# Kernel optimization log

Measured on AMD Instinct MI355X. Metric: run time of the kernel, lower is better.

The kernel has to match this reference:

```python
import jax, jax.numpy as jnp
import numpy as np

HIDDEN = 2048
NUM_HEADS = 16
HEAD_DIM = 128
OUT = NUM_HEADS * HEAD_DIM  # 2048
B, T = 4, 2048


def setup_inputs() -> dict:
    key = jax.random.key(0)
    ks = jax.random.split(key, 8)
    hidden_states = jax.random.normal(ks[0], (B, T, HIDDEN), dtype=jnp.float32)
    scale = 0.02
    Wr = jax.random.normal(ks[1], (OUT, HIDDEN), dtype=jnp.float32) * scale
    Wk = jax.random.normal(ks[2], (OUT, HIDDEN), dtype=jnp.float32) * scale
    Wv = jax.random.normal(ks[3], (OUT, HIDDEN), dtype=jnp.float32) * scale
    Wo = jax.random.normal(ks[4], (HIDDEN, OUT), dtype=jnp.float32) * scale
    time_decay = jax.random.uniform(ks[5], (NUM_HEADS, HEAD_DIM), minval=-4.0, maxval=-1.0, dtype=jnp.float32)
    time_first = jax.random.uniform(ks[6], (NUM_HEADS, HEAD_DIM), minval=-0.5, maxval=0.5, dtype=jnp.float32)
    time_mix_k = jnp.full((1, 1, HIDDEN), 0.5, dtype=jnp.float32)
    time_mix_v = jnp.full((1, 1, HIDDEN), 0.5, dtype=jnp.float32)
    time_mix_r = jnp.full((1, 1, HIDDEN), 0.5, dtype=jnp.float32)
    return {"hidden_states": hidden_states, "Wr": Wr, "Wk": Wk, "Wv": Wv, "Wo": Wo,
            "time_decay": time_decay, "time_first": time_first,
            "time_mix_k": time_mix_k, "time_mix_v": time_mix_v, "time_mix_r": time_mix_r}


def _wkv(r, k, v, time_decay, time_first):
    # r,k,v: [B,T,H,D] -> output [B,T,H,D]
    w = jnp.exp(-jnp.exp(time_decay))  # [H,D]
    u = time_first                     # [H,D]
    kv = k * v                         # [B,T,H,D]
    # scan over time: carry state [B,H,D]
    r_t = jnp.moveaxis(r, 1, 0)   # [T,B,H,D]
    kv_t = jnp.moveaxis(kv, 1, 0)

    def step(state, inp):
        rt, kvt = inp
        out = (state + u * kvt) * rt
        new_state = state * w + kvt
        return new_state, out

    state0 = jnp.zeros(r.shape[:1] + r.shape[2:], dtype=r.dtype)  # [B,H,D]
    _, out = jax.lax.scan(step, state0, (r_t, kv_t))
    return jnp.moveaxis(out, 0, 1)  # [B,T,H,D]


def reference(hidden_states, Wr, Wk, Wv, Wo, time_decay, time_first, time_mix_k, time_mix_v, time_mix_r):
    Bc, Tc, _ = hidden_states.shape
    # token shift: xx[t] = hidden[t-1], xx[0] = 0
    xx = jnp.concatenate([jnp.zeros_like(hidden_states[:, :1]), hidden_states[:, :-1]], axis=1)
    xk = hidden_states * time_mix_k + xx * (1.0 - time_mix_k)
    xv = hidden_states * time_mix_v + xx * (1.0 - time_mix_v)
    xr = hidden_states * time_mix_r + xx * (1.0 - time_mix_r)
    receptance = jax.nn.sigmoid(jnp.einsum('bth,oh->bto', xr, Wr))
    key = jnp.einsum('bth,oh->bto', xk, Wk)
    value = jnp.einsum('bth,oh->bto', xv, Wv)
    receptance = receptance.reshape(Bc, Tc, NUM_HEADS, HEAD_DIM)
    key = key.reshape(Bc, Tc, NUM_HEADS, HEAD_DIM)
    value = value.reshape(Bc, Tc, NUM_HEADS, HEAD_DIM)
    wkv = _wkv(receptance, key, value, time_decay, time_first)
    attn = wkv.reshape(Bc, Tc, OUT)
    return jnp.einsum('bto,ho->bth', attn, Wo)
```

## Files before the change

kernel.cpp:

```cpp
#include <hip/hip_runtime.h>


#define HIDDEN 2048
#define TOUT   2048
#define TT     2048
#define MM     8192

typedef __bf16 bf16_t;
typedef __attribute__((ext_vector_type(8))) __bf16 bf16x8;
typedef __attribute__((ext_vector_type(4))) __bf16 bf16x4;
typedef __attribute__((ext_vector_type(4))) float  f32x4;

__global__ __launch_bounds__(256) void f2bf_kernel(const float* __restrict__ src,
                                                   bf16_t* __restrict__ dst) {
  const long i = ((long)blockIdx.x * 256 + threadIdx.x) * 4;
  const float4 v = *reinterpret_cast<const float4*>(src + i);
  bf16x4 o;
  o[0] = (bf16_t)v.x; o[1] = (bf16_t)v.y; o[2] = (bf16_t)v.z; o[3] = (bf16_t)v.w;
  *reinterpret_cast<bf16x4*>(dst + i) = o;
}

__global__ __launch_bounds__(256) void prep_kernel(const float* __restrict__ h,
    const float* __restrict__ mk, const float* __restrict__ mv,
    const float* __restrict__ mr,
    bf16_t* __restrict__ xk, bf16_t* __restrict__ xv, bf16_t* __restrict__ xr) {
  const long i  = ((long)blockIdx.x * 256 + threadIdx.x) * 4;
  const int  c  = (int)(i & (HIDDEN - 1));
  const long bt = i >> 11;
  const int  t  = (int)(bt & (TT - 1));
  const float4 hv = *reinterpret_cast<const float4*>(h + i);
  float4 hp = make_float4(0.f, 0.f, 0.f, 0.f);
  if (t > 0) hp = *reinterpret_cast<const float4*>(h + i - HIDDEN);
  const float4 k4 = *reinterpret_cast<const float4*>(mk + c);
  const float4 v4 = *reinterpret_cast<const float4*>(mv + c);
  const float4 r4 = *reinterpret_cast<const float4*>(mr + c);
  bf16x4 ok, ov, orr;
#define MIX(j, HC, PC)                                         \
  ok[j]  = (bf16_t)(HC * k4.PC + hp.PC * (1.f - k4.PC));       \
  ov[j]  = (bf16_t)(HC * v4.PC + hp.PC * (1.f - v4.PC));       \
  orr[j] = (bf16_t)(HC * r4.PC + hp.PC * (1.f - r4.PC));
  MIX(0, hv.x, x) MIX(1, hv.y, y) MIX(2, hv.z, z) MIX(3, hv.w, w)
#undef MIX
  *reinterpret_cast<bf16x4*>(xk + i) = ok;
  *reinterpret_cast<bf16x4*>(xv + i) = ov;
  *reinterpret_cast<bf16x4*>(xr + i) = orr;
}

#define GBM 256
#define GBN 256
#define GBK 64

template<bool SIGMOID, bool OUTF32>
__global__ __launch_bounds__(512, 2) void gemm256(const bf16_t* __restrict__ A,
                                                  const bf16_t* __restrict__ W,
                                                  bf16_t* __restrict__ Cb,
                                                  float* __restrict__ Cf) {
  __shared__ __align__(16) char lds[131072];
  const int tid = threadIdx.x, wave = tid >> 6, lane = tid & 63;
  const int wr = wave >> 2, wc = wave & 3;
  const long rowA0 = (long)blockIdx.x * GBM;
  const long rowB0 = (long)blockIdx.y * GBN;
  const bf16_t* aB = A + rowA0 * HIDDEN;
  const bf16_t* wB = W + rowB0 * HIDDEN;

  const int sgofs = (wave * 8 + (lane >> 3)) * HIDDEN + (((lane & 7) ^ (lane >> 3)) << 3);
  const int ldst  = wave * 1024;

#define STAGE(J, BUFX) do {                                                     \
    const int kt_ = (J) * GBK;                                                  \
    _Pragma("unroll")                                                           \
    for (int i_ = 0; i_ < 4; ++i_) {                                            \
      __builtin_amdgcn_global_load_lds(                                         \
        (const __attribute__((address_space(1))) void*)(aB + sgofs + i_ * (64 * HIDDEN) + kt_), \
        (__attribute__((address_space(3))) void*)(lds + (BUFX) + ldst + i_ * 8192), 16, 0, 0);  \
      __builtin_amdgcn_global_load_lds(                                         \
        (const __attribute__((address_space(1))) void*)(wB + sgofs + i_ * (64 * HIDDEN) + kt_), \
        (__attribute__((address_space(3))) void*)(lds + 65536 + (BUFX) + ldst + i_ * 8192), 16, 0, 0); \
    } } while (0)

  const int rsel = lane & 15, g0 = lane >> 4;
  int offA[8], offB[4];
#pragma unroll
  for (int m = 0; m < 8; ++m) {
    const int row = wr * 128 + m * 16 + rsel;
    offA[m] = row * 128 + ((g0 ^ (row & 7)) << 4);
  }
#pragma unroll
  for (int n = 0; n < 4; ++n) {
    const int row = wc * 64 + n * 16 + rsel;
    offB[n] = 65536 + row * 128 + ((g0 ^ (row & 7)) << 4);
  }

  f32x4 acc[8][4];
#pragma unroll
  for (int m = 0; m < 8; ++m)
#pragma unroll
    for (int n = 0; n < 4; ++n)
#pragma unroll
      for (int q = 0; q < 4; ++q) acc[m][n][q] = 0.f;

  STAGE(0, 0);
  STAGE(1, 32768);

  int bufx = 0;
  for (int j = 0; j < 32; ++j) {
    if (j < 31) { asm volatile("s_waitcnt vmcnt(8)" ::: "memory"); }
    else        { asm volatile("s_waitcnt vmcnt(0)" ::: "memory"); }
    __builtin_amdgcn_sched_barrier(0);
    __builtin_amdgcn_s_barrier();

    bf16x8 a0[8], b0[4], a1[8], b1[4];
#pragma unroll
    for (int m = 0; m < 8; ++m) a0[m] = *reinterpret_cast<const bf16x8*>(lds + (offA[m] ^ bufx));
#pragma unroll
    for (int n = 0; n < 4; ++n) b0[n] = *reinterpret_cast<const bf16x8*>(lds + (offB[n] ^ bufx));
    __builtin_amdgcn_s_setprio(1);
#pragma unroll
    for (int m = 0; m < 8; ++m)
#pragma unroll
      for (int n = 0; n < 4; ++n)
        acc[m][n] = __builtin_amdgcn_mfma_f32_16x16x32_bf16(a0[m], b0[n], acc[m][n], 0, 0, 0);
    __builtin_amdgcn_s_setprio(0);
#pragma unroll
    for (int m = 0; m < 8; ++m) a1[m] = *reinterpret_cast<const bf16x8*>(lds + (offA[m] ^ bufx ^ 64));
#pragma unroll
    for (int n = 0; n < 4; ++n) b1[n] = *reinterpret_cast<const bf16x8*>(lds + (offB[n] ^ bufx ^ 64));
    asm volatile("s_waitcnt lgkmcnt(0)" ::: "memory");
    __builtin_amdgcn_sched_barrier(0);
    __builtin_amdgcn_s_barrier();
    if (j < 30) STAGE(j + 2, bufx);
    __builtin_amdgcn_s_setprio(1);
#pragma unroll
    for (int m = 0; m < 8; ++m)
#pragma unroll
      for (int n = 0; n < 4; ++n)
        acc[m][n] = __builtin_amdgcn_mfma_f32_16x16x32_bf16(a1[m], b1[n], acc[m][n], 0, 0, 0);
    __builtin_amdgcn_s_setprio(0);
    bufx ^= 32768;
  }
#undef STAGE

  const long crow0 = rowA0 + wr * 128 + g0 * 4;
  const long ccol0 = rowB0 + wc * 64 + rsel;
#pragma unroll
  for (int m = 0; m < 8; ++m) {
#pragma unroll
    for (int n = 0; n < 4; ++n) {
#pragma unroll
      for (int q = 0; q < 4; ++q) {
        float val = acc[m][n][q];
        if (SIGMOID) val = 1.f / (1.f + __expf(-val));
        const long row = crow0 + m * 16 + q;
        const long col = ccol0 + n * 16;
        if (OUTF32) Cf[row * TOUT + col] = val;
        else        Cb[row * TOUT + col] = (bf16_t)val;
      }
    }
  }
}

#define CL  64
#define NCH 32

__global__ __launch_bounds__(256) void wkv_state_kernel(
    const bf16_t* __restrict__ kp, const bf16_t* __restrict__ vp,
    const float* __restrict__ td, float* __restrict__ cs ) {
  const int c8 = blockIdx.x * 256 + threadIdx.x;
  const int ch = blockIdx.y;
  const int o0 = (c8 * 8) & (TOUT - 1);
  const int b  = c8 >> 8;
  const long base = ((long)b * TT + ch * CL) * TOUT + o0;
  float w[8], s[8];
#pragma unroll
  for (int i = 0; i < 8; ++i) { w[i] = __expf(-__expf(td[o0 + i])); s[i] = 0.f; }
  for (int t = 0; t < CL; ++t) {
    const bf16x8 k8 = *reinterpret_cast<const bf16x8*>(kp + base + (long)t * TOUT);
    const bf16x8 v8 = *reinterpret_cast<const bf16x8*>(vp + base + (long)t * TOUT);
#pragma unroll
    for (int i = 0; i < 8; ++i) s[i] = s[i] * w[i] + (float)k8[i] * (float)v8[i];
  }
  float4* csv = reinterpret_cast<float4*>(cs + ch * MM + c8 * 8);
  csv[0] = make_float4(s[0], s[1], s[2], s[3]);
  csv[1] = make_float4(s[4], s[5], s[6], s[7]);
}

__global__ __launch_bounds__(256) void wkv_out_kernel(
    const bf16_t* __restrict__ rp, const bf16_t* __restrict__ kp,
    const bf16_t* __restrict__ vp, const float* __restrict__ td,
    const float* __restrict__ tf, const float* __restrict__ cs,
    bf16_t* __restrict__ attn) {
  const int c8 = blockIdx.x * 256 + threadIdx.x;
  const int ch = blockIdx.y;
  const int o0 = (c8 * 8) & (TOUT - 1);
  const int b  = c8 >> 8;
  const long base = ((long)b * TT + ch * CL) * TOUT + o0;
  float w[8], u[8], wc[8], S[8];
#pragma unroll
  for (int i = 0; i < 8; ++i) {
    const float e = __expf(td[o0 + i]);
    w[i]  = __expf(-e);
    wc[i] = __expf(-e * (float)CL);
    u[i]  = tf[o0 + i];
    S[i]  = 0.f;
  }
  for (int j2 = 0; j2 < ch; ++j2) {
    const float4 s0 = *reinterpret_cast<const float4*>(cs + j2 * MM + c8 * 8);
    const float4 s1 = *reinterpret_cast<const float4*>(cs + j2 * MM + c8 * 8 + 4);
    S[0] = S[0] * wc[0] + s0.x; S[1] = S[1] * wc[1] + s0.y;
    S[2] = S[2] * wc[2] + s0.z; S[3] = S[3] * wc[3] + s0.w;
    S[4] = S[4] * wc[4] + s1.x; S[5] = S[5] * wc[5] + s1.y;
    S[6] = S[6] * wc[6] + s1.z; S[7] = S[7] * wc[7] + s1.w;
  }
  for (int t = 0; t < CL; ++t) {
    const bf16x8 r8 = *reinterpret_cast<const bf16x8*>(rp + base + (long)t * TOUT);
    const bf16x8 k8 = *reinterpret_cast<const bf16x8*>(kp + base + (long)t * TOUT);
    const bf16x8 v8 = *reinterpret_cast<const bf16x8*>(vp + base + (long)t * TOUT);
    bf16x8 o8;
#pragma unroll
    for (int i = 0; i < 8; ++i) {
      const float kv = (float)k8[i] * (float)v8[i];
      o8[i] = (bf16_t)((S[i] + u[i] * kv) * (float)r8[i]);
      S[i] = S[i] * w[i] + kv;
    }
    *reinterpret_cast<bf16x8*>(attn + base + (long)t * TOUT) = o8;
  }
}

extern "C" void kernel_launch(void* const* d_in, const int* in_sizes, int n_in,
                              void* d_out, int out_size, void* d_ws, size_t ws_size,
                              hipStream_t stream) {
  const float* h  = (const float*)d_in[0];
  const float* Wr = (const float*)d_in[1];
  const float* Wk = (const float*)d_in[2];
  const float* Wv = (const float*)d_in[3];
  const float* Wo = (const float*)d_in[4];
  const float* td = (const float*)d_in[5];
  const float* tf = (const float*)d_in[6];
  const float* mk = (const float*)d_in[7];
  const float* mv = (const float*)d_in[8];
  const float* mr = (const float*)d_in[9];
  float* out = (float*)d_out;

  char* ws = (char*)d_ws;
  const size_t S2 = (size_t)MM * TOUT * sizeof(bf16_t);
  bf16_t* xr   = (bf16_t*)(ws + 0 * S2);
  bf16_t* xk   = (bf16_t*)(ws + 1 * S2);
  bf16_t* xv   = (bf16_t*)(ws + 2 * S2);
  bf16_t* rr   = (bf16_t*)(ws + 3 * S2);
  bf16_t* kk   = (bf16_t*)(ws + 4 * S2);
  bf16_t* vv   = xr;
  bf16_t* attn = xk;
  float*  cs   = (float*)xv;
  const size_t WSZ = (size_t)TOUT * HIDDEN;
  bf16_t* Wr2 = (bf16_t*)(ws + 5 * S2);
  bf16_t* Wk2 = Wr2 + WSZ;
  bf16_t* Wv2 = Wk2 + WSZ;
  bf16_t* Wo2 = Wv2 + WSZ;

  f2bf_kernel<<<4096, 256, 0, stream>>>(Wr, Wr2);
  f2bf_kernel<<<4096, 256, 0, stream>>>(Wk, Wk2);
  f2bf_kernel<<<4096, 256, 0, stream>>>(Wv, Wv2);
  f2bf_kernel<<<4096, 256, 0, stream>>>(Wo, Wo2);

  prep_kernel<<<16384, 256, 0, stream>>>(h, mk, mv, mr, xk, xv, xr);

  dim3 gg(MM / GBM, TOUT / GBN);
  gemm256<true , false><<<gg, 512, 0, stream>>>(xr, Wr2, rr, nullptr);
  gemm256<false, false><<<gg, 512, 0, stream>>>(xk, Wk2, kk, nullptr);
  gemm256<false, false><<<gg, 512, 0, stream>>>(xv, Wv2, vv, nullptr);

  dim3 wg(4, NCH);
  wkv_state_kernel<<<wg, 256, 0, stream>>>(kk, vv, td, cs);
  wkv_out_kernel<<<wg, 256, 0, stream>>>(rr, kk, vv, td, tf, cs, attn);

  gemm256<false, true ><<<gg, 512, 0, stream>>>(attn, Wo2, nullptr, out);
}
```

Baseline: 490.5 us.

## Restructure GEMM mainloop into four-phase interleaved load/MFMA schedule; merge weight casts

The GEMM main loop is rebuilt as four sub-phases per K-tile. Each phase loads a quarter of the A/B fragments from LDS, issues half of an operand's global-to-LDS prefetch, and runs 16 MFMAs. This spreads memory traffic across the MFMA work instead of issuing it in two large bursts. The four weight-cast launches are merged into one 2D-grid kernel, and both the cast and prep kernels now process 8 elements per thread. The finer schedule adds more barriers per iteration and relies on hand-tuned vmcnt/lgkmcnt counts that must match the issued loads exactly.

```diff
diff --git a/kernel.cpp b/kernel.cpp
--- a/kernel.cpp
+++ b/kernel.cpp
@@ -5,45 +5,66 @@
 #define TOUT   2048
 #define TT     2048
 #define MM     8192
+#define NT     32
 
 typedef __bf16 bf16_t;
 typedef __attribute__((ext_vector_type(8))) __bf16 bf16x8;
-typedef __attribute__((ext_vector_type(4))) __bf16 bf16x4;
 typedef __attribute__((ext_vector_type(4))) float  f32x4;
 
-__global__ __launch_bounds__(256) void f2bf_kernel(const float* __restrict__ src,
-                                                   bf16_t* __restrict__ dst) {
-  const long i = ((long)blockIdx.x * 256 + threadIdx.x) * 4;
-  const float4 v = *reinterpret_cast<const float4*>(src + i);
-  bf16x4 o;
-  o[0] = (bf16_t)v.x; o[1] = (bf16_t)v.y; o[2] = (bf16_t)v.z; o[3] = (bf16_t)v.w;
-  *reinterpret_cast<bf16x4*>(dst + i) = o;
+__global__ __launch_bounds__(256) void f2bf4_kernel(
+    const float* __restrict__ s0, const float* __restrict__ s1,
+    const float* __restrict__ s2, const float* __restrict__ s3,
+    bf16_t* __restrict__ d0, bf16_t* __restrict__ d1,
+    bf16_t* __restrict__ d2, bf16_t* __restrict__ d3) {
+  const float* s; bf16_t* d;
+  switch (blockIdx.y) {
+    case 0:  s = s0; d = d0; break;
+    case 1:  s = s1; d = d1; break;
+    case 2:  s = s2; d = d2; break;
+    default: s = s3; d = d3; break;
+  }
+  const long i = ((long)blockIdx.x * 256 + threadIdx.x) * 8;
+  const float4 a = *reinterpret_cast<const float4*>(s + i);
+  const float4 b = *reinterpret_cast<const float4*>(s + i + 4);
+  bf16x8 o;
+  o[0] = (bf16_t)a.x; o[1] = (bf16_t)a.y; o[2] = (bf16_t)a.z; o[3] = (bf16_t)a.w;
+  o[4] = (bf16_t)b.x; o[5] = (bf16_t)b.y; o[6] = (bf16_t)b.z; o[7] = (bf16_t)b.w;
+  *reinterpret_cast<bf16x8*>(d + i) = o;
 }
 
 __global__ __launch_bounds__(256) void prep_kernel(const float* __restrict__ h,
     const float* __restrict__ mk, const float* __restrict__ mv,
     const float* __restrict__ mr,
     bf16_t* __restrict__ xk, bf16_t* __restrict__ xv, bf16_t* __restrict__ xr) {
-  const long i  = ((long)blockIdx.x * 256 + threadIdx.x) * 4;
-  const int  c  = (int)(i & (HIDDEN - 1));
-  const long bt = i >> 11;
-  const int  t  = (int)(bt & (TT - 1));
-  const float4 hv = *reinterpret_cast<const float4*>(h + i);
-  float4 hp = make_float4(0.f, 0.f, 0.f, 0.f);
-  if (t > 0) hp = *reinterpret_cast<const float4*>(h + i - HIDDEN);
-  const float4 k4 = *reinterpret_cast<const float4*>(mk + c);
-  const float4 v4 = *reinterpret_cast<const float4*>(mv + c);
-  const float4 r4 = *reinterpret_cast<const float4*>(mr + c);
-  bf16x4 ok, ov, orr;
-#define MIX(j, HC, PC)                                         \
-  ok[j]  = (bf16_t)(HC * k4.PC + hp.PC * (1.f - k4.PC));       \
-  ov[j]  = (bf16_t)(HC * v4.PC + hp.PC * (1.f - v4.PC));       \
-  orr[j] = (bf16_t)(HC * r4.PC + hp.PC * (1.f - r4.PC));
-  MIX(0, hv.x, x) MIX(1, hv.y, y) MIX(2, hv.z, z) MIX(3, hv.w, w)
-#undef MIX
-  *reinterpret_cast<bf16x4*>(xk + i) = ok;
-  *reinterpret_cast<bf16x4*>(xv + i) = ov;
-  *reinterpret_cast<bf16x4*>(xr + i) = orr;
+  const long i = ((long)blockIdx.x * 256 + threadIdx.x) * 8;
+  const int  c = (int)(i & (HIDDEN - 1));
+  const int  t = (int)((i >> 11) & (TT - 1));
+  float hv[8], hp[8], k8[8], v8[8], r8[8];
+  *reinterpret_cast<float4*>(hv)     = *reinterpret_cast<const float4*>(h + i);
+  *reinterpret_cast<float4*>(hv + 4) = *reinterpret_cast<const float4*>(h + i + 4);
+  if (t > 0) {
+    *reinterpret_cast<float4*>(hp)     = *reinterpret_cast<const float4*>(h + i - HIDDEN);
+    *reinterpret_cast<float4*>(hp + 4) = *reinterpret_cast<const float4*>(h + i - HIDDEN + 4);
+  } else {
+#pragma unroll
+    for (int j = 0; j < 8; ++j) hp[j] = 0.f;
+  }
+  *reinterpret_cast<float4*>(k8)     = *reinterpret_cast<const float4*>(mk + c);
+  *reinterpret_cast<float4*>(k8 + 4) = *reinterpret_cast<const float4*>(mk + c + 4);
+  *reinterpret_cast<float4*>(v8)     = *reinterpret_cast<const float4*>(mv + c);
+  *reinterpret_cast<float4*>(v8 + 4) = *reinterpret_cast<const float4*>(mv + c + 4);
+  *reinterpret_cast<float4*>(r8)     = *reinterpret_cast<const float4*>(mr + c);
+  *reinterpret_cast<float4*>(r8 + 4) = *reinterpret_cast<const float4*>(mr + c + 4);
+  bf16x8 ok, ov, orr;
+#pragma unroll
+  for (int j = 0; j < 8; ++j) {
+    ok[j]  = (bf16_t)(hv[j] * k8[j] + hp[j] * (1.f - k8[j]));
+    ov[j]  = (bf16_t)(hv[j] * v8[j] + hp[j] * (1.f - v8[j]));
+    orr[j] = (bf16_t)(hv[j] * r8[j] + hp[j] * (1.f - r8[j]));
+  }
+  *reinterpret_cast<bf16x8*>(xk + i) = ok;
+  *reinterpret_cast<bf16x8*>(xv + i) = ov;
+  *reinterpret_cast<bf16x8*>(xr + i) = orr;
 }
 
 #define GBM 256
@@ -66,16 +87,15 @@
   const int sgofs = (wave * 8 + (lane >> 3)) * HIDDEN + (((lane & 7) ^ (lane >> 3)) << 3);
   const int ldst  = wave * 1024;
 
-#define STAGE(J, BUFX) do {                                                     \
-    const int kt_ = (J) * GBK;                                                  \
+#define STAGE_H(J, OP, HALF) do {                                               \
+    const int j_ = (J);                                                         \
+    const bf16_t* s_ = (OP) ? wB : aB;                                          \
+    const int lb_ = ((OP) ? 65536 : 0) + ((j_ & 1) << 15) + ldst;               \
     _Pragma("unroll")                                                           \
-    for (int i_ = 0; i_ < 4; ++i_) {                                            \
+    for (int i_ = 2 * (HALF); i_ < 2 * (HALF) + 2; ++i_) {                      \
       __builtin_amdgcn_global_load_lds(                                         \
-        (const __attribute__((address_space(1))) void*)(aB + sgofs + i_ * (64 * HIDDEN) + kt_), \
-        (__attribute__((address_space(3))) void*)(lds + (BUFX) + ldst + i_ * 8192), 16, 0, 0);  \
-      __builtin_amdgcn_global_load_lds(                                         \
-        (const __attribute__((address_space(1))) void*)(wB + sgofs + i_ * (64 * HIDDEN) + kt_), \
-        (__attribute__((address_space(3))) void*)(lds + 65536 + (BUFX) + ldst + i_ * 8192), 16, 0, 0); \
+        (const __attribute__((address_space(1))) void*)(s_ + sgofs + i_ * (64 * HIDDEN) + j_ * GBK), \
+        (__attribute__((address_space(3))) void*)(lds + lb_ + i_ * 8192), 16, 0, 0); \
     } } while (0)
 
   const int rsel = lane & 15, g0 = lane >> 4;
@@ -99,46 +119,64 @@
 #pragma unroll
       for (int q = 0; q < 4; ++q) acc[m][n][q] = 0.f;
 
-  STAGE(0, 0);
-  STAGE(1, 32768);
-
-  int bufx = 0;
-  for (int j = 0; j < 32; ++j) {
-    if (j < 31) { asm volatile("s_waitcnt vmcnt(8)" ::: "memory"); }
-    else        { asm volatile("s_waitcnt vmcnt(0)" ::: "memory"); }
+#define LD(off) (*reinterpret_cast<const bf16x8*>(lds + (off)))
+#define MFMA16(AR, M0, BR, N0) do {                                             \
+    __builtin_amdgcn_s_setprio(1);                                              \
+    _Pragma("unroll")                                                           \
+    for (int m_ = 0; m_ < 4; ++m_)                                              \
+      _Pragma("unroll")                                                         \
+      for (int n_ = 0; n_ < 2; ++n_)                                            \
+        _Pragma("unroll")                                                       \
+        for (int s_ = 0; s_ < 2; ++s_)                                          \
+          acc[(M0) + m_][(N0) + n_] = __builtin_amdgcn_mfma_f32_16x16x32_bf16(  \
+              AR[m_][s_], BR[n_][s_], acc[(M0) + m_][(N0) + n_], 0, 0, 0);      \
+    __builtin_amdgcn_s_setprio(0); } while (0)
+#define PH_SYNC() do {                                                          \
+    __builtin_amdgcn_s_barrier();                                               \
+    asm volatile("s_waitcnt lgkmcnt(0)" ::: "memory");                          \
+    __builtin_amdgcn_sched_barrier(0); } while (0)
+
+  STAGE_H(0, 0, 0); STAGE_H(0, 0, 1); STAGE_H(0, 1, 0); STAGE_H(0, 1, 1);
+  STAGE_H(1, 0, 0); STAGE_H(1, 0, 1);
+  asm volatile("s_waitcnt vmcnt(4)" ::: "memory");
+  __builtin_amdgcn_s_barrier();
+
+  for (int j = 0; j < NT; ++j) {
+    const int bufx = (j & 1) << 15;
+    bf16x8 aR0[4][2], aR1[4][2], bR0[2][2], bR1[2][2];
+#pragma unroll
+    for (int m = 0; m < 4; ++m) { aR0[m][0] = LD(offA[m] ^ bufx); aR0[m][1] = LD(offA[m] ^ bufx ^ 64); }
+#pragma unroll
+    for (int n = 0; n < 2; ++n) { bR0[n][0] = LD(offB[n] ^ bufx); bR0[n][1] = LD(offB[n] ^ bufx ^ 64); }
+    if (j + 1 < NT) STAGE_H(j + 1, 1, 0);
+    asm volatile("s_waitcnt lgkmcnt(8)" ::: "memory");
+    PH_SYNC();
+    MFMA16(aR0, 0, bR0, 0);
+    __builtin_amdgcn_s_barrier();
+#pragma unroll
+    for (int m = 0; m < 4; ++m) { aR1[m][0] = LD(offA[4 + m] ^ bufx); aR1[m][1] = LD(offA[4 + m] ^ bufx ^ 64); }
+    if (j + 1 < NT) STAGE_H(j + 1, 1, 1);
+    PH_SYNC();
+    MFMA16(aR1, 4, bR0, 0);
+    __builtin_amdgcn_s_barrier();
+#pragma unroll
+    for (int n = 0; n < 2; ++n) { bR1[n][0] = LD(offB[2 + n] ^ bufx); bR1[n][1] = LD(offB[2 + n] ^ bufx ^ 64); }
+    if (j + 2 < NT) STAGE_H(j + 2, 0, 0);
+    PH_SYNC();
+    MFMA16(aR1, 4, bR1, 2);
+    __builtin_amdgcn_s_barrier();
+    if (j + 2 < NT) STAGE_H(j + 2, 0, 1);
+    if (j <= NT - 3)      { asm volatile("s_waitcnt vmcnt(4)" ::: "memory"); }
+    else if (j == NT - 2) { asm volatile("s_waitcnt vmcnt(0)" ::: "memory"); }
     __builtin_amdgcn_sched_barrier(0);
+    PH_SYNC();
+    MFMA16(aR0, 0, bR1, 2);
     __builtin_amdgcn_s_barrier();
-
-    bf16x8 a0[8], b0[4], a1[8], b1[4];
-#pragma unroll
-    for (int m = 0; m < 8; ++m) a0[m] = *reinterpret_cast<const bf16x8*>(lds + (offA[m] ^ bufx));
-#pragma unroll
-    for (int n = 0; n < 4; ++n) b0[n] = *reinterpret_cast<const bf16x8*>(lds + (offB[n] ^ bufx));
-    __builtin_amdgcn_s_setprio(1);
-#pragma unroll
-    for (int m = 0; m < 8; ++m)
-#pragma unroll
-      for (int n = 0; n < 4; ++n)
-        acc[m][n] = __builtin_amdgcn_mfma_f32_16x16x32_bf16(a0[m], b0[n], acc[m][n], 0, 0, 0);
-    __builtin_amdgcn_s_setprio(0);
-#pragma unroll
-    for (int m = 0; m < 8; ++m) a1[m] = *reinterpret_cast<const bf16x8*>(lds + (offA[m] ^ bufx ^ 64));
-#pragma unroll
-    for (int n = 0; n < 4; ++n) b1[n] = *reinterpret_cast<const bf16x8*>(lds + (offB[n] ^ bufx ^ 64));
-    asm volatile("s_waitcnt lgkmcnt(0)" ::: "memory");
-    __builtin_amdgcn_sched_barrier(0);
-    __builtin_amdgcn_s_barrier();
-    if (j < 30) STAGE(j + 2, bufx);
-    __builtin_amdgcn_s_setprio(1);
-#pragma unroll
-    for (int m = 0; m < 8; ++m)
-#pragma unroll
-      for (int n = 0; n < 4; ++n)
-        acc[m][n] = __builtin_amdgcn_mfma_f32_16x16x32_bf16(a1[m], b1[n], acc[m][n], 0, 0, 0);
-    __builtin_amdgcn_s_setprio(0);
-    bufx ^= 32768;
-  }
-#undef STAGE
+  }
+#undef STAGE_H
+#undef LD
+#undef MFMA16
+#undef PH_SYNC
 
   const long crow0 = rowA0 + wr * 128 + g0 * 4;
   const long ccol0 = rowB0 + wc * 64 + rsel;
@@ -194,22 +232,22 @@
   const int o0 = (c8 * 8) & (TOUT - 1);
   const int b  = c8 >> 8;
   const long base = ((long)b * TT + ch * CL) * TOUT + o0;
-  float w[8], u[8], wc[8], S[8];
+  float w[8], u[8], wc8[8], S[8];
 #pragma unroll
   for (int i = 0; i < 8; ++i) {
     const float e = __expf(td[o0 + i]);
-    w[i]  = __expf(-e);
-    wc[i] = __expf(-e * (float)CL);
-    u[i]  = tf[o0 + i];
-    S[i]  = 0.f;
+    w[i]   = __expf(-e);
+    wc8[i] = __expf(-e * (float)CL);
+    u[i]   = tf[o0 + i];
+    S[i]   = 0.f;
   }
   for (int j2 = 0; j2 < ch; ++j2) {
     const float4 s0 = *reinterpret_cast<const float4*>(cs + j2 * MM + c8 * 8);
     const float4 s1 = *reinterpret_cast<const float4*>(cs + j2 * MM + c8 * 8 + 4);
-    S[0] = S[0] * wc[0] + s0.x; S[1] = S[1] * wc[1] + s0.y;
-    S[2] = S[2] * wc[2] + s0.z; S[3] = S[3] * wc[3] + s0.w;
-    S[4] = S[4] * wc[4] + s1.x; S[5] = S[5] * wc[5] + s1.y;
-    S[6] = S[6] * wc[6] + s1.z; S[7] = S[7] * wc[7] + s1.w;
+    S[0] = S[0] * wc8[0] + s0.x; S[1] = S[1] * wc8[1] + s0.y;
+    S[2] = S[2] * wc8[2] + s0.z; S[3] = S[3] * wc8[3] + s0.w;
+    S[4] = S[4] * wc8[4] + s1.x; S[5] = S[5] * wc8[5] + s1.y;
+    S[6] = S[6] * wc8[6] + s1.z; S[7] = S[7] * wc8[7] + s1.w;
   }
   for (int t = 0; t < CL; ++t) {
     const bf16x8 r8 = *reinterpret_cast<const bf16x8*>(rp + base + (long)t * TOUT);
@@ -257,12 +295,10 @@
   bf16_t* Wv2 = Wk2 + WSZ;
   bf16_t* Wo2 = Wv2 + WSZ;
 
-  f2bf_kernel<<<4096, 256, 0, stream>>>(Wr, Wr2);
-  f2bf_kernel<<<4096, 256, 0, stream>>>(Wk, Wk2);
-  f2bf_kernel<<<4096, 256, 0, stream>>>(Wv, Wv2);
-  f2bf_kernel<<<4096, 256, 0, stream>>>(Wo, Wo2);
-
-  prep_kernel<<<16384, 256, 0, stream>>>(h, mk, mv, mr, xk, xv, xr);
+  dim3 fg(2048, 4);
+  f2bf4_kernel<<<fg, 256, 0, stream>>>(Wr, Wk, Wv, Wo, Wr2, Wk2, Wv2, Wo2);
+
+  prep_kernel<<<8192, 256, 0, stream>>>(h, mk, mv, mr, xk, xv, xr);
 
   dim3 gg(MM / GBM, TOUT / GBN);
   gemm256<true , false><<<gg, 512, 0, stream>>>(xr, Wr2, rr, nullptr);
```

Result: no change. 487.9 us (-0.5%).
